# Performance work log

Measured on AMD Instinct MI355X. Metric: run time of the kernel, lower is better.

Reference implementation:

```python
import jax, jax.numpy as jnp
import numpy as np

jax.config.update("jax_enable_x64", True)

EPS = 1e-6
NUM_LEVELS = 16
LOG2_T = 19
BASE_RES = 16
DESIRED_RES = 2048
F = 2
N_POINTS = 131072
PS = (1, 19349663, 83492791)
CORNERS = np.array([[0, 0, 0], [0, 0, 1], [0, 1, 0], [0, 1, 1],
                    [1, 0, 0], [1, 0, 1], [1, 1, 0], [1, 1, 1]], dtype=np.float32)


def _isprime(n):
    if n < 2:
        return False
    i = 2
    while i * i <= n:
        if n % i == 0:
            return False
        i += 1
    return True


def _build_meta():
    T = 2 ** LOG2_T
    while not _isprime(T):
        T += 1
    b = (DESIRED_RES / BASE_RES) ** (1.0 / (NUM_LEVELS - 1))
    offsets = [0]
    scales = []
    start_hash = -1
    for i in range(NUM_LEVELS):
        res = int(BASE_RES * b ** i)
        scales.append(res)
        n = (res + 1) ** 3
        if n > T:
            if start_hash < 0:
                start_hash = i
            n = T
        offsets.append(offsets[-1] + n)
    sh = NUM_LEVELS if start_hash == -1 else start_hash
    return T, np.array(scales, dtype=np.int64), np.array(offsets, dtype=np.int64), sh


TABLE, SCALES, OFFSETS, START_HASH = _build_meta()


def setup_inputs():
    key = jax.random.key(0)
    k1, k2 = jax.random.split(key)
    xyz = jax.random.normal(k1, (N_POINTS, 3), dtype=jnp.float32)
    wbounds = jnp.arange(6, dtype=jnp.float32)  # box min [0,1,2], max [3,4,5]
    std = 1e-4
    data = jax.random.uniform(k2, (int(OFFSETS[-1]), F), dtype=jnp.float32,
                              minval=-std, maxval=std)
    return {"xyz": xyz, "wbounds": wbounds, "data": data}


def _hashgrid(xyz, wbounds, data):
    scales_f = jnp.asarray(SCALES, dtype=jnp.float32)   # [L]
    scales_i = jnp.asarray(SCALES)                      # [L] int64
    corner = jnp.asarray(CORNERS)                       # [8,3] float32
    level_off = jnp.asarray(OFFSETS[:-1])               # [L] int64
    # normalize into [0,1]^3 (torch uses .item() on the max -> detached)
    x = jnp.clip(xyz, wbounds[:3], wbounds[3:6])
    denom = jax.lax.stop_gradient(jnp.max(wbounds[3:6] - wbounds[:3])) + EPS
    x = (x - wbounds[:3]) / denom
    fx = x[None] * scales_f[:, None, None]              # [L,N,3]
    int_xyz = (fx[:, :, None, :] + corner[None, None]).astype(jnp.int64)  # [L,N,8,3]
    off = fx - int_xyz[:, :, 0].astype(jnp.float32)     # [L,N,3] frac part
    sp1 = scales_i + 1
    dense = (int_xyz[..., 0] * (sp1 ** 2)[:, None, None]
             + int_xyz[..., 1] * sp1[:, None, None]
             + int_xyz[..., 2])                          # [L,N,8]
    hashed = ((int_xyz[..., 0] * PS[0]) ^ (int_xyz[..., 1] * PS[1])
              ^ (int_xyz[..., 2] * PS[2])) % TABLE       # [L,N,8]
    lvl = jnp.arange(NUM_LEVELS, dtype=jnp.int64)[:, None, None]
    ind = jnp.where(lvl < START_HASH, dense, hashed) + level_off[:, None, None]
    val = data[ind]                                      # [L,N,8,F] gather
    # trilinear weights per corner
    w = jnp.clip(1.0 - corner[None, None]
                 + (2.0 * corner[None, None] - 1.0) * off[:, :, None, :], 0.0, 1.0)
    wprod = w[..., 0] * w[..., 1] * w[..., 2]            # [L,N,8]
    out = jnp.einsum('lnc,lncf->lnf', wprod, val)        # [L,N,F]
    return out.transpose(1, 0, 2).reshape(-1, NUM_LEVELS * F)


def reference(xyz, wbounds, data):
    return _hashgrid(xyz, wbounds, data)
```

## Files before the change

### kernel.cpp

```cpp
#include <hip/hip_runtime.h>
#include <stdint.h>
#include <math.h>

#define NLVL 16
#define NPTS 131072

struct Meta {
  int scales[NLVL];
  int offsets[NLVL];
  unsigned int T;
  int start_hash;
  double invT;
};

__device__ __forceinline__ int fastmod(uint64_t h, unsigned int T, double invT) {
  uint64_t q = (uint64_t)((double)h * invT);
  long long r = (long long)(h - q * (uint64_t)T);
  if (r < 0) r += (long long)T;
  else if (r >= (long long)T) r -= (long long)T;
  return (int)r;
}

__device__ __forceinline__ void level_idx(
    int l, float xn, float yn, float zn, const Meta& m,
    int* __restrict__ idx, float* __restrict__ o)
{
#pragma clang fp contract(off)
  const float sf = (float)m.scales[l];
  const float fx = xn * sf, fy = yn * sf, fz = zn * sf;
  const int ix0 = (int)fx,          iy0 = (int)fy,          iz0 = (int)fz;
  const int ix1 = (int)(fx + 1.0f), iy1 = (int)(fy + 1.0f), iz1 = (int)(fz + 1.0f);
  o[0] = fx - (float)ix0; o[1] = fy - (float)iy0; o[2] = fz - (float)iz0;
  const int base = m.offsets[l];

  if (l < m.start_hash) {
    const int sp1 = m.scales[l] + 1;
    const int sq  = sp1 * sp1;
    const int ax0 = ix0 * sq,  ax1 = ix1 * sq;
    const int ay0 = iy0 * sp1, ay1 = iy1 * sp1;
    idx[0] = base + ax0 + ay0 + iz0;
    idx[1] = base + ax0 + ay0 + iz1;
    idx[2] = base + ax0 + ay1 + iz0;
    idx[3] = base + ax0 + ay1 + iz1;
    idx[4] = base + ax1 + ay0 + iz0;
    idx[5] = base + ax1 + ay0 + iz1;
    idx[6] = base + ax1 + ay1 + iz0;
    idx[7] = base + ax1 + ay1 + iz1;
  } else {
    const uint64_t hx0 = (uint64_t)ix0;
    const uint64_t hx1 = (uint64_t)ix1;
    const uint64_t hy0 = (uint64_t)iy0 * 19349663ull;
    const uint64_t hy1 = hy0 + 19349663ull;
    const uint64_t hz0 = (uint64_t)iz0 * 83492791ull;
    const uint64_t hz1 = hz0 + 83492791ull;
    idx[0] = base + fastmod(hx0 ^ hy0 ^ hz0, m.T, m.invT);
    idx[1] = base + fastmod(hx0 ^ hy0 ^ hz1, m.T, m.invT);
    idx[2] = base + fastmod(hx0 ^ hy1 ^ hz0, m.T, m.invT);
    idx[3] = base + fastmod(hx0 ^ hy1 ^ hz1, m.T, m.invT);
    idx[4] = base + fastmod(hx1 ^ hy0 ^ hz0, m.T, m.invT);
    idx[5] = base + fastmod(hx1 ^ hy0 ^ hz1, m.T, m.invT);
    idx[6] = base + fastmod(hx1 ^ hy1 ^ hz0, m.T, m.invT);
    idx[7] = base + fastmod(hx1 ^ hy1 ^ hz1, m.T, m.invT);
  }
}

__device__ __forceinline__ void accum8(
    const float2* __restrict__ v, const float* __restrict__ o,
    float& a0, float& a1)
{
#pragma clang fp contract(off)
  const float wx[2] = {1.0f - o[0], o[0]};
  const float wy[2] = {1.0f - o[1], o[1]};
  const float wz[2] = {1.0f - o[2], o[2]};
  a0 = 0.0f; a1 = 0.0f;
#pragma unroll
  for (int c = 0; c < 8; ++c) {
    const float w = (wx[(c >> 2) & 1] * wy[(c >> 1) & 1]) * wz[c & 1];
    a0 += w * v[c].x;
    a1 += w * v[c].y;
  }
}

__global__ __launch_bounds__(256) void hashgrid_fwd(
    const float* __restrict__ xyz,
    const float* __restrict__ wb,
    const float* __restrict__ data,
    float* __restrict__ out,
    Meta meta)
{
#pragma clang fp contract(off)
  const int c    = threadIdx.x;
  const int hc   = c >> 5;
  const int pc   = c & 31;
  const int base = blockIdx.x * 32;

  __shared__ float sxyz[96];
  if (c < 96) sxyz[c] = xyz[base * 3 + c];
  __syncthreads();

  const float bx0 = wb[0], by0 = wb[1], bz0 = wb[2];
  const float bx1 = wb[3], by1 = wb[4], bz1 = wb[5];
  const float denom = fmaxf(fmaxf(bx1 - bx0, by1 - by0), bz1 - bz0) + 1e-6f;

  float px = sxyz[pc * 3 + 0], py = sxyz[pc * 3 + 1], pz = sxyz[pc * 3 + 2];
  px = fminf(fmaxf(px, bx0), bx1);
  py = fminf(fmaxf(py, by0), by1);
  pz = fminf(fmaxf(pz, bz0), bz1);
  const float xn = (px - bx0) / denom;
  const float yn = (py - by0) / denom;
  const float zn = (pz - bz0) / denom;

  const int lA = hc * 2, lB = hc * 2 + 1;
  int idxA[8], idxB[8];
  float oA[3], oB[3];
  level_idx(lA, xn, yn, zn, meta, idxA, oA);
  level_idx(lB, xn, yn, zn, meta, idxB, oB);

  const float2* __restrict__ dp = (const float2*)data;
  float2 vA[8], vB[8];
#pragma unroll
  for (int k = 0; k < 8; ++k) vA[k] = dp[idxA[k]];
#pragma unroll
  for (int k = 0; k < 8; ++k) vB[k] = dp[idxB[k]];

  float4 r;
  accum8(vA, oA, r.x, r.y);
  accum8(vB, oB, r.z, r.w);

  __shared__ float4 lds[32][9];
  lds[pc][hc] = r;
  __syncthreads();

  const int p2 = c >> 3, h2 = c & 7;
  const float4 v = lds[p2][h2];
  reinterpret_cast<float4*>(out)[(base + p2) * 8 + h2] = v;
}

static bool isprime_ll(long long v) {
  if (v < 2) return false;
  for (long long i = 2; i * i <= v; ++i)
    if (v % i == 0) return false;
  return true;
}

extern "C" void kernel_launch(void* const* d_in, const int* in_sizes, int n_in,
                              void* d_out, int out_size, void* d_ws, size_t ws_size,
                              hipStream_t stream) {
  (void)in_sizes; (void)n_in; (void)d_ws; (void)ws_size; (void)out_size;

  Meta m;
  long long T = 1LL << 19;
  while (!isprime_ll(T)) ++T;
  const double b = pow(2048.0 / 16.0, 1.0 / 15.0);
  long long off = 0;
  int sh = -1;
  for (int i = 0; i < NLVL; ++i) {
    const int res = (int)(16.0 * pow(b, (double)i));
    m.scales[i] = res;
    m.offsets[i] = (int)off;
    long long nn = (long long)(res + 1) * (res + 1) * (res + 1);
    if (nn > T) { if (sh < 0) sh = i; nn = T; }
    off += nn;
  }
  m.T = (unsigned int)T;
  m.start_hash = (sh < 0) ? NLVL : sh;
  m.invT = 1.0 / (double)T;

  const float* xyz  = (const float*)d_in[0];
  const float* wbp  = (const float*)d_in[1];
  const float* data = (const float*)d_in[2];
  float* out = (float*)d_out;

  hipLaunchKernelGGL(hashgrid_fwd, dim3(NPTS / 32), dim3(256), 0, stream,
                     xyz, wbp, data, out, m);
}
```

Baseline: 40.38 us.

## Map level pairs to XCDs so each XCD's L2 holds only its levels' tables

Changes the work split so each block handles 256 points for one fixed pair of levels (group and group+8). The group is taken from blockIdx modulo 8, so with round-robin block dispatch each XCD always touches the same two level tables. This is meant to shrink each XCD's L2 working set and cut gather misses. In exchange, output stores become strided 8-byte writes that are no longer coalesced, and the xyz chunk is loaded eight times.

```diff
diff --git a/kernel.cpp b/kernel.cpp
--- a/kernel.cpp
+++ b/kernel.cpp
@@ -4,6 +4,8 @@
 
 #define NLVL 16
 #define NPTS 131072
+#define CHUNK 256
+#define NXCD 8
 
 struct Meta {
   int scales[NLVL];
@@ -89,20 +91,23 @@
     Meta meta)
 {
 #pragma clang fp contract(off)
-  const int c    = threadIdx.x;
-  const int hc   = c >> 5;
-  const int pc   = c & 31;
-  const int base = blockIdx.x * 32;
+  const int c     = threadIdx.x;
+  const int group = blockIdx.x & (NXCD - 1);
+  const int chunk = blockIdx.x >> 3;
+  const int pbase = chunk * CHUNK;
 
-  __shared__ float sxyz[96];
-  if (c < 96) sxyz[c] = xyz[base * 3 + c];
+  __shared__ float sxyz[CHUNK * 3];
+  if (c < CHUNK * 3 / 4) {
+    reinterpret_cast<float4*>(sxyz)[c] =
+        reinterpret_cast<const float4*>(xyz + pbase * 3)[c];
+  }
   __syncthreads();
 
   const float bx0 = wb[0], by0 = wb[1], bz0 = wb[2];
   const float bx1 = wb[3], by1 = wb[4], bz1 = wb[5];
   const float denom = fmaxf(fmaxf(bx1 - bx0, by1 - by0), bz1 - bz0) + 1e-6f;
 
-  float px = sxyz[pc * 3 + 0], py = sxyz[pc * 3 + 1], pz = sxyz[pc * 3 + 2];
+  float px = sxyz[c * 3 + 0], py = sxyz[c * 3 + 1], pz = sxyz[c * 3 + 2];
   px = fminf(fmaxf(px, bx0), bx1);
   py = fminf(fmaxf(py, by0), by1);
   pz = fminf(fmaxf(pz, bz0), bz1);
@@ -110,7 +115,7 @@
   const float yn = (py - by0) / denom;
   const float zn = (pz - bz0) / denom;
 
-  const int lA = hc * 2, lB = hc * 2 + 1;
+  const int lA = group, lB = group + 8;
   int idxA[8], idxB[8];
   float oA[3], oB[3];
   level_idx(lA, xn, yn, zn, meta, idxA, oA);
@@ -123,17 +128,14 @@
 #pragma unroll
   for (int k = 0; k < 8; ++k) vB[k] = dp[idxB[k]];
 
-  float4 r;
-  accum8(vA, oA, r.x, r.y);
-  accum8(vB, oB, r.z, r.w);
+  float2 rA, rB;
+  accum8(vA, oA, rA.x, rA.y);
+  accum8(vB, oB, rB.x, rB.y);
 
-  __shared__ float4 lds[32][9];
-  lds[pc][hc] = r;
-  __syncthreads();
-
-  const int p2 = c >> 3, h2 = c & 7;
-  const float4 v = lds[p2][h2];
-  reinterpret_cast<float4*>(out)[(base + p2) * 8 + h2] = v;
+  float2* __restrict__ o2 = reinterpret_cast<float2*>(out);
+  const int pt = pbase + c;
+  o2[pt * NLVL + lA] = rA;
+  o2[pt * NLVL + lB] = rB;
 }
 
 static bool isprime_ll(long long v) {
@@ -171,6 +173,6 @@
   const float* data = (const float*)d_in[2];
   float* out = (float*)d_out;
 
-  hipLaunchKernelGGL(hashgrid_fwd, dim3(NPTS / 32), dim3(256), 0, stream,
-                     xyz, wbp, data, out, m);
+  hipLaunchKernelGGL(hashgrid_fwd, dim3((NPTS / CHUNK) * NXCD), dim3(256), 0,
+                     stream, xyz, wbp, data, out, m);
 }
```

Measured after the change: 46.37 us. 1.15x slower.

## Spatially sort block points into coarse cells and give each wave four levels

Applied to the files above, without the earlier changes.

Each block now handles 64 points instead of 32. The points are bucketed into a 4x4x4 coarse grid with a shared-memory histogram, prefix scan and scatter, so that the lanes of a wave process spatially nearby points. Each wave then covers four levels in a loop, one point per lane, instead of two levels over 32 points. The intent is better locality and coalescing of the gathers in dense levels, plus fewer blocks. The cost is extra sync and atomic overhead and a serial level loop per thread.

```diff
diff --git a/kernel.cpp b/kernel.cpp
--- a/kernel.cpp
+++ b/kernel.cpp
@@ -4,6 +4,8 @@
 
 #define NLVL 16
 #define NPTS 131072
+#define BPTS 64
+#define NTHR 256
 
 struct Meta {
   int scales[NLVL];
@@ -64,24 +66,7 @@
   }
 }
 
-__device__ __forceinline__ void accum8(
-    const float2* __restrict__ v, const float* __restrict__ o,
-    float& a0, float& a1)
-{
-#pragma clang fp contract(off)
-  const float wx[2] = {1.0f - o[0], o[0]};
-  const float wy[2] = {1.0f - o[1], o[1]};
-  const float wz[2] = {1.0f - o[2], o[2]};
-  a0 = 0.0f; a1 = 0.0f;
-#pragma unroll
-  for (int c = 0; c < 8; ++c) {
-    const float w = (wx[(c >> 2) & 1] * wy[(c >> 1) & 1]) * wz[c & 1];
-    a0 += w * v[c].x;
-    a1 += w * v[c].y;
-  }
-}
-
-__global__ __launch_bounds__(256) void hashgrid_fwd(
+__global__ __launch_bounds__(NTHR) void hashgrid_fwd(
     const float* __restrict__ xyz,
     const float* __restrict__ wb,
     const float* __restrict__ data,
@@ -89,20 +74,62 @@
     Meta meta)
 {
 #pragma clang fp contract(off)
-  const int c    = threadIdx.x;
-  const int hc   = c >> 5;
-  const int pc   = c & 31;
-  const int base = blockIdx.x * 32;
-
-  __shared__ float sxyz[96];
-  if (c < 96) sxyz[c] = xyz[base * 3 + c];
+  const int t    = threadIdx.x;
+  const int wave = t >> 6;
+  const int lane = t & 63;
+  const int pbase = blockIdx.x * BPTS;
+
+  __shared__ float  sxyz[BPTS * 3];
+  __shared__ int    hist[64];
+  __shared__ int    sidx[BPTS];
+  __shared__ float2 tile[BPTS][NLVL + 1];
+
+  if (t < 48)
+    reinterpret_cast<float4*>(sxyz)[t] =
+        reinterpret_cast<const float4*>(xyz + pbase * 3)[t];
+  if (t < 64) hist[t] = 0;
   __syncthreads();
 
   const float bx0 = wb[0], by0 = wb[1], bz0 = wb[2];
   const float bx1 = wb[3], by1 = wb[4], bz1 = wb[5];
   const float denom = fmaxf(fmaxf(bx1 - bx0, by1 - by0), bz1 - bz0) + 1e-6f;
 
-  float px = sxyz[pc * 3 + 0], py = sxyz[pc * 3 + 1], pz = sxyz[pc * 3 + 2];
+  int key = 0;
+  if (t < 64) {
+    float px = sxyz[t * 3 + 0], py = sxyz[t * 3 + 1], pz = sxyz[t * 3 + 2];
+    px = fminf(fmaxf(px, bx0), bx1);
+    py = fminf(fmaxf(py, by0), by1);
+    pz = fminf(fmaxf(pz, bz0), bz1);
+    const float xn = (px - bx0) / denom;
+    const float yn = (py - by0) / denom;
+    const float zn = (pz - bz0) / denom;
+    const int kx = min((int)(xn * 4.0f), 3);
+    const int ky = min((int)(yn * 4.0f), 3);
+    const int kz = min((int)(zn * 4.0f), 3);
+    key = kx * 16 + ky * 4 + kz;
+    atomicAdd(&hist[key], 1);
+  }
+  __syncthreads();
+
+  if (t < 64) {
+    int v = hist[t];
+#pragma unroll
+    for (int d = 1; d < 64; d <<= 1) {
+      int u = __shfl_up(v, d, 64);
+      if (lane >= d) v += u;
+    }
+    hist[t] = v;
+  }
+  __syncthreads();
+
+  if (t < 64) {
+    const int pos = atomicSub(&hist[key], 1) - 1;
+    sidx[pos] = t;
+  }
+  __syncthreads();
+
+  const int p = sidx[lane];
+  float px = sxyz[p * 3 + 0], py = sxyz[p * 3 + 1], pz = sxyz[p * 3 + 2];
   px = fminf(fmaxf(px, bx0), bx1);
   py = fminf(fmaxf(py, by0), by1);
   pz = fminf(fmaxf(pz, bz0), bz1);
@@ -110,30 +137,43 @@
   const float yn = (py - by0) / denom;
   const float zn = (pz - bz0) / denom;
 
-  const int lA = hc * 2, lB = hc * 2 + 1;
-  int idxA[8], idxB[8];
-  float oA[3], oB[3];
-  level_idx(lA, xn, yn, zn, meta, idxA, oA);
-  level_idx(lB, xn, yn, zn, meta, idxB, oB);
-
   const float2* __restrict__ dp = (const float2*)data;
-  float2 vA[8], vB[8];
-#pragma unroll
-  for (int k = 0; k < 8; ++k) vA[k] = dp[idxA[k]];
-#pragma unroll
-  for (int k = 0; k < 8; ++k) vB[k] = dp[idxB[k]];
-
-  float4 r;
-  accum8(vA, oA, r.x, r.y);
-  accum8(vB, oB, r.z, r.w);
-
-  __shared__ float4 lds[32][9];
-  lds[pc][hc] = r;
-  __syncthreads();
-
-  const int p2 = c >> 3, h2 = c & 7;
-  const float4 v = lds[p2][h2];
-  reinterpret_cast<float4*>(out)[(base + p2) * 8 + h2] = v;
+
+#pragma unroll 2
+  for (int s = 0; s < 4; ++s) {
+    const int l = wave + 4 * s;
+    int idx[8];
+    float o[3];
+    level_idx(l, xn, yn, zn, meta, idx, o);
+
+    float2 v[8];
+#pragma unroll
+    for (int k = 0; k < 8; ++k) v[k] = dp[idx[k]];
+
+    const float wx[2] = {1.0f - o[0], o[0]};
+    const float wy[2] = {1.0f - o[1], o[1]};
+    const float wz[2] = {1.0f - o[2], o[2]};
+    float a0 = 0.0f, a1 = 0.0f;
+#pragma unroll
+    for (int c = 0; c < 8; ++c) {
+      const float w = (wx[(c >> 2) & 1] * wy[(c >> 1) & 1]) * wz[c & 1];
+      a0 += w * v[c].x;
+      a1 += w * v[c].y;
+    }
+    tile[p][l] = make_float2(a0, a1);
+  }
+  __syncthreads();
+
+#pragma unroll
+  for (int it = 0; it < 2; ++it) {
+    const int idx = t + it * NTHR;
+    const int pp = idx >> 3;
+    const int q  = idx & 7;
+    const float2 e0 = tile[pp][2 * q];
+    const float2 e1 = tile[pp][2 * q + 1];
+    reinterpret_cast<float4*>(out)[(pbase + pp) * 8 + q] =
+        make_float4(e0.x, e0.y, e1.x, e1.y);
+  }
 }
 
 static bool isprime_ll(long long v) {
@@ -171,6 +211,6 @@
   const float* data = (const float*)d_in[2];
   float* out = (float*)d_out;
 
-  hipLaunchKernelGGL(hashgrid_fwd, dim3(NPTS / 32), dim3(256), 0, stream,
+  hipLaunchKernelGGL(hashgrid_fwd, dim3(NPTS / BPTS), dim3(NTHR), 0, stream,
                      xyz, wbp, data, out, m);
 }
```

Result: faster. 32.54 us (-19.4%).
